# Kernel tuning notes

Measured on AMD Instinct MI355X. Metric: run time of the kernel, lower is better.

## Reference

```python
import jax, jax.numpy as jnp
import numpy as np

EPSILON = 1e-6
B, I, H, C, S = 131072, 64, 128, 16, 3  # batch, input_size, hidden_size, num_channels, spatial dim


def _linear_w(key, fan_in, fan_out):
    # torch.nn.Linear default init: U(-1/sqrt(fan_in), 1/sqrt(fan_in)); stored as [in, out] for x @ W
    bound = 1.0 / np.sqrt(fan_in)
    return jax.random.uniform(key, (fan_in, fan_out), jnp.float32, -bound, bound)


def setup_inputs() -> dict:
    key = jax.random.key(0)
    ks = jax.random.split(key, 11)
    return {
        "invariant_input": jax.random.normal(ks[0], (B, I), jnp.float32),
        "equivariant_input": jax.random.normal(ks[1], (B, S), jnp.float32),
        "invariant_hidden": jax.random.normal(ks[2], (B, H), jnp.float32),
        "equivariant_hidden": jax.random.normal(ks[3], (B, S, C), jnp.float32),
        # DotProductProjection(1+C -> H), no bias
        "W_left": _linear_w(ks[4], 1 + C, H),
        "W_right": _linear_w(ks[5], 1 + C, H),
        # invariant_to_invariant: Linear(I+H -> H) with bias
        "W_ii": _linear_w(ks[6], I + H, H),
        "b_ii": jax.random.uniform(ks[7], (H,), jnp.float32, -1.0 / np.sqrt(I + H), 1.0 / np.sqrt(I + H)),
        # equivariant_to_equivariant: Linear(1+C -> C), no bias
        "W_ee": _linear_w(ks[8], 1 + C, C),
        # Damping fc: Linear(I+H -> C), no bias
        "W_damp": _linear_w(ks[9], I + H, C),
    }


def reference(invariant_input, equivariant_input, invariant_hidden, equivariant_hidden,
              W_left, W_right, W_ii, b_ii, W_ee, W_damp):
    # eq_comb: [B, S, 1+C]; inv_comb: [B, I+H]
    eq_comb = jnp.concatenate([equivariant_input[..., None], equivariant_hidden], axis=-1)
    inv_comb = jnp.concatenate([invariant_input, invariant_hidden], axis=-1)

    # DotProductProjection (x1 = x0): normalize by squared-norm over spatial dim, project, dot over spatial dim
    norm = jnp.sum(eq_comb * eq_comb, axis=-2, keepdims=True) + EPSILON  # [B, 1, 1+C]
    xn = eq_comb / norm                                                  # [B, S, 1+C]
    proj = jnp.sum((xn @ W_left) * (xn @ W_right), axis=-2)              # [B, H]

    new_invariant = jnp.tanh(proj + inv_comb @ W_ii + b_ii)              # [B, H]

    # Damping: equivariant state gated by an invariant-derived per-channel factor
    gate = (inv_comb @ W_damp)[..., None, :]                             # [B, 1, C]
    new_equivariant = eq_comb @ W_ee + equivariant_hidden * gate         # [B, S, C]

    return (new_invariant, new_equivariant)
```

## Files before the change

kernel.cpp:

```cpp
#include <hip/hip_runtime.h>


typedef _Float16 half8  __attribute__((ext_vector_type(8)));
typedef _Float16 half4v __attribute__((ext_vector_type(4)));
typedef float    float4v __attribute__((ext_vector_type(4)));

#define MFMA16(A, Bv, C) __builtin_amdgcn_mfma_f32_16x16x32_f16((A), (Bv), (C), 0, 0, 0)

#define N_TILES 8192
#define GRID    2048

__global__ __launch_bounds__(256, 2) void rye_elman_kernel(
    const float* __restrict__ inv_in,
    const float* __restrict__ eq_in,
    const float* __restrict__ inv_hid,
    const float* __restrict__ eq_hid,
    const float* __restrict__ Wl_g,
    const float* __restrict__ Wr_g,
    const float* __restrict__ Wii_g,
    const float* __restrict__ bii_g,
    const float* __restrict__ Wee_g,
    const float* __restrict__ Wd_g,
    float* __restrict__ out0,
    float* __restrict__ out1)
{
    __shared__ __align__(16) _Float16 A_ii[16][200];
    __shared__ __align__(16) _Float16 A_xn[16][136];
    __shared__ __align__(16) _Float16 A_rw[16][136];
    __shared__ float eqin_s[16][3];
    __shared__ __align__(16) float eh_s[16][48];
    __shared__ __align__(16) float proj_s[16][132];
    __shared__ float ee_s[16][52];
    __shared__ float gate_s[16][16];

    const int tid  = threadIdx.x;
    const int w    = tid >> 6;
    const int lane = tid & 63;
    const int q    = lane >> 4;
    const int m    = lane & 15;

    {
        unsigned* z0 = (unsigned*)&A_xn[0][0];
        unsigned* z1 = (unsigned*)&A_rw[0][0];
        for (int i = tid; i < 16 * 136 / 2; i += 256) { z0[i] = 0u; z1[i] = 0u; }
    }

    half8 wii[2][6], wl[2], wr[2], wdamp[6], wee;
    float biiv[2];
#pragma unroll
    for (int t = 0; t < 2; ++t) {
        const int col = 32 * w + 16 * t + m;
        biiv[t] = bii_g[col];
#pragma unroll
        for (int s = 0; s < 6; ++s) {
            half8 u;
#pragma unroll
            for (int j = 0; j < 8; ++j)
                u[j] = (_Float16)Wii_g[(32 * s + 8 * q + j) * 128 + col];
            wii[t][s] = u;
        }
        half8 ul, ur;
#pragma unroll
        for (int j = 0; j < 8; ++j) {
            const int k = 8 * q + j;
            ul[j] = (k < 17) ? (_Float16)Wl_g[k * 128 + col] : (_Float16)0.f;
            ur[j] = (k < 17) ? (_Float16)Wr_g[k * 128 + col] : (_Float16)0.f;
        }
        wl[t] = ul; wr[t] = ur;
    }
#pragma unroll
    for (int s = 0; s < 6; ++s) {
        half8 u;
#pragma unroll
        for (int j = 0; j < 8; ++j)
            u[j] = (_Float16)Wd_g[(32 * s + 8 * q + j) * 16 + m];
        wdamp[s] = u;
    }
    {
        half8 u;
#pragma unroll
        for (int j = 0; j < 8; ++j) {
            const int k = 8 * q + j;
            u[j] = (k < 17) ? (_Float16)Wee_g[k * 16 + m] : (_Float16)0.f;
        }
        wee = u;
    }
    __syncthreads();

    float4 p_inv, p_hid0, p_hid1, p_eh;
    float  p_eq;

#define LOAD_TILE(BASE)                                                     \
    do {                                                                    \
        const long _b = (BASE);                                             \
        p_inv  = ((const float4*)(inv_in  + _b * 64))[tid];                 \
        p_hid0 = ((const float4*)(inv_hid + _b * 128))[tid];                \
        p_hid1 = ((const float4*)(inv_hid + _b * 128))[tid + 256];          \
        if (tid < 192) p_eh = ((const float4*)(eq_hid + _b * 48))[tid];     \
        if (tid < 48)  p_eq = eq_in[_b * 3 + tid];                          \
    } while (0)

    LOAD_TILE((long)blockIdx.x * 16);

    for (int tile = blockIdx.x; tile < N_TILES; tile += GRID) {
        const long base = (long)tile * 16;

        if (tid < 48) eqin_s[tid / 3][tid % 3] = p_eq;
        if (tid < 192) *(float4*)&eh_s[tid / 12][(tid % 12) * 4] = p_eh;
        {
            half4v h; h[0] = (_Float16)p_inv.x; h[1] = (_Float16)p_inv.y;
                      h[2] = (_Float16)p_inv.z; h[3] = (_Float16)p_inv.w;
            *(half4v*)&A_ii[tid >> 4][(tid & 15) * 4] = h;
        }
        {
            half4v h; h[0] = (_Float16)p_hid0.x; h[1] = (_Float16)p_hid0.y;
                      h[2] = (_Float16)p_hid0.z; h[3] = (_Float16)p_hid0.w;
            *(half4v*)&A_ii[tid >> 5][64 + (tid & 31) * 4] = h;
            const int i1 = tid + 256;
            half4v g; g[0] = (_Float16)p_hid1.x; g[1] = (_Float16)p_hid1.y;
                      g[2] = (_Float16)p_hid1.z; g[3] = (_Float16)p_hid1.w;
            *(half4v*)&A_ii[i1 >> 5][64 + (i1 & 31) * 4] = g;
        }
        __syncthreads();

        if (tile + GRID < N_TILES) LOAD_TILE((long)(tile + GRID) * 16);

        for (int t = tid; t < 816; t += 256) {
            const int r = t / 51, rem = t % 51;
            const int s = rem / 17, c = rem % 17;
            float x0, x1, x2;
            if (c == 0) { x0 = eqin_s[r][0]; x1 = eqin_s[r][1]; x2 = eqin_s[r][2]; }
            else        { x0 = eh_s[r][c - 1]; x1 = eh_s[r][15 + c]; x2 = eh_s[r][31 + c]; }
            const float a  = fmaf(x0, x0, fmaf(x1, x1, fmaf(x2, x2, 1e-6f)));
            const float rn = __builtin_amdgcn_rcpf(a);
            const float x  = (s == 0) ? x0 : (s == 1) ? x1 : x2;
            A_rw[r][s * 32 + c] = (_Float16)x;
            A_xn[r][s * 32 + c] = (_Float16)(x * rn);
        }
        __syncthreads();

        float4v acc[2] = {{0.f,0.f,0.f,0.f},{0.f,0.f,0.f,0.f}};
        float4v accg   = {0.f,0.f,0.f,0.f};
#pragma unroll
        for (int s = 0; s < 6; ++s) {
            half8 a = *(const half8*)&A_ii[m][8 * q + 32 * s];
            acc[0] = MFMA16(a, wii[0][s], acc[0]);
            acc[1] = MFMA16(a, wii[1][s], acc[1]);
            if (w == 0) accg = MFMA16(a, wdamp[s], accg);
        }
        const float4v z4 = {0.f,0.f,0.f,0.f};
#pragma unroll
        for (int g = 0; g < 4; ++g) {
            const int arow = 4 * g + (m >> 2);
            const int aoff = (m & 3) * 32 + 8 * q;
            half8 ax = *(const half8*)&A_xn[arow][aoff];
#pragma unroll
            for (int t = 0; t < 2; ++t) {
                float4v L = MFMA16(ax, wl[t], z4);
                float4v R = MFMA16(ax, wr[t], z4);
                proj_s[4 * g + q][32 * w + 16 * t + m] =
                    L[0]*R[0] + L[1]*R[1] + L[2]*R[2];
            }
            if (w == 1) {
                half8 ar = *(const half8*)&A_rw[arow][aoff];
                float4v E = MFMA16(ar, wee, z4);
                ee_s[4 * g + q][m]      = E[0];
                ee_s[4 * g + q][16 + m] = E[1];
                ee_s[4 * g + q][32 + m] = E[2];
            }
        }
        if (w == 0) {
#pragma unroll
            for (int r = 0; r < 4; ++r) gate_s[4 * q + r][m] = accg[r];
        }
        __syncthreads();

#pragma unroll
        for (int t = 0; t < 2; ++t) {
            const int col = 32 * w + 16 * t + m;
#pragma unroll
            for (int r = 0; r < 4; ++r) {
                const float x = acc[t][r] + proj_s[4 * q + r][col] + biiv[t];
                const float e = __expf(2.f * x);
                proj_s[4 * q + r][col] = 1.f - 2.f * __builtin_amdgcn_rcpf(e + 1.f);
            }
        }
        for (int i = tid; i < 768; i += 256) {
            const int b = i / 48, j = i % 48;
            out1[base * 48 + i] = ee_s[b][j] + eh_s[b][j] * gate_s[b][j & 15];
        }
        __syncthreads();

        {
            const long ob = base * 128;
#pragma unroll
            for (int h = 0; h < 2; ++h) {
                const int idx = (tid + 256 * h) * 4;
                const int r = idx >> 7, c = idx & 127;
                float4 v = *(const float4*)&proj_s[r][c];
                *(float4*)&out0[ob + idx] = v;
            }
        }
    }
#undef LOAD_TILE
}

extern "C" void kernel_launch(void* const* d_in, const int* in_sizes, int n_in,
                              void* d_out, int out_size, void* d_ws, size_t ws_size,
                              hipStream_t stream) {
    const float* inv_in  = (const float*)d_in[0];
    const float* eq_in   = (const float*)d_in[1];
    const float* inv_hid = (const float*)d_in[2];
    const float* eq_hid  = (const float*)d_in[3];
    const float* Wl      = (const float*)d_in[4];
    const float* Wr      = (const float*)d_in[5];
    const float* Wii     = (const float*)d_in[6];
    const float* bii     = (const float*)d_in[7];
    const float* Wee     = (const float*)d_in[8];
    const float* Wd      = (const float*)d_in[9];
    float* o0 = (float*)d_out;
    float* o1 = o0 + (size_t)131072 * 128;
    hipLaunchKernelGGL(rye_elman_kernel, dim3(GRID), dim3(256), 0, stream,
                       inv_in, eq_in, inv_hid, eq_hid, Wl, Wr, Wii, bii, Wee, Wd, o0, o1);
}
```

Before: 247.1 us.

## Restructure to one wave per 16-row tile with weights staged in LDS

Each wave now processes its own 16-row tile. The weights are converted to fp16 once per block and held in transposed, padded LDS buffers instead of registers. Activations are loaded straight from global memory into MFMA operand registers, which removes the per-tile LDS staging and all block-level barriers inside the tile loop. Outputs are written directly from the MFMA results, trading coalesced float4 stores for scattered scalar stores and dropping the software prefetch of the next tile. The block size becomes 512 threads with a grid of 512 blocks.

```diff
diff --git a/kernel.cpp b/kernel.cpp
--- a/kernel.cpp
+++ b/kernel.cpp
@@ -2,15 +2,17 @@
 
 
 typedef _Float16 half8  __attribute__((ext_vector_type(8)));
-typedef _Float16 half4v __attribute__((ext_vector_type(4)));
 typedef float    float4v __attribute__((ext_vector_type(4)));
 
-#define MFMA16(A, Bv, C) __builtin_amdgcn_mfma_f32_16x16x32_f16((A), (Bv), (C), 0, 0, 0)
+#define MFMA16(A, B, C) __builtin_amdgcn_mfma_f32_16x16x32_f16((A), (B), (C), 0, 0, 0)
 
-#define N_TILES 8192
-#define GRID    2048
+#define WII_P 200
+#define WLR_P 40
+#define NTILES 8192
+#define NBLOCKS 512
+#define NWAVES (NBLOCKS * 8)
 
-__global__ __launch_bounds__(256, 2) void rye_elman_kernel(
+__global__ __launch_bounds__(512, 4) void rye_elman_kernel(
     const float* __restrict__ inv_in,
     const float* __restrict__ eq_in,
     const float* __restrict__ inv_hid,
@@ -24,185 +26,155 @@
     float* __restrict__ out0,
     float* __restrict__ out1)
 {
-    __shared__ __align__(16) _Float16 A_ii[16][200];
-    __shared__ __align__(16) _Float16 A_xn[16][136];
-    __shared__ __align__(16) _Float16 A_rw[16][136];
-    __shared__ float eqin_s[16][3];
-    __shared__ __align__(16) float eh_s[16][48];
-    __shared__ __align__(16) float proj_s[16][132];
-    __shared__ float ee_s[16][52];
-    __shared__ float gate_s[16][16];
+    __shared__ __align__(16) _Float16 Wii_t[128 * WII_P];
+    __shared__ __align__(16) _Float16 Wl_t [128 * WLR_P];
+    __shared__ __align__(16) _Float16 Wr_t [128 * WLR_P];
+    __shared__ __align__(16) _Float16 Wd_t [ 16 * WII_P];
+    __shared__ __align__(16) _Float16 We_t [ 16 * WLR_P];
+    __shared__ float bii_s[128];
 
-    const int tid  = threadIdx.x;
-    const int w    = tid >> 6;
+    const int tid = threadIdx.x;
+
+    for (int i = tid; i < 128 * WLR_P; i += 512) { Wl_t[i] = (_Float16)0.f; Wr_t[i] = (_Float16)0.f; }
+    for (int i = tid; i < 16 * WLR_P; i += 512)  We_t[i] = (_Float16)0.f;
+    __syncthreads();
+    for (int i = tid; i < 192 * 128; i += 512) {
+        const int k = i >> 7, c = i & 127;
+        Wii_t[c * WII_P + k] = (_Float16)Wii_g[i];
+    }
+    for (int i = tid; i < 17 * 128; i += 512) {
+        const int r = i >> 7, c = i & 127, sl = (r == 0) ? 16 : r - 1;
+        Wl_t[c * WLR_P + sl] = (_Float16)Wl_g[i];
+        Wr_t[c * WLR_P + sl] = (_Float16)Wr_g[i];
+    }
+    for (int i = tid; i < 192 * 16; i += 512) {
+        const int k = i >> 4, c = i & 15;
+        Wd_t[c * WII_P + k] = (_Float16)Wd_g[i];
+    }
+    for (int i = tid; i < 17 * 16; i += 512) {
+        const int r = i >> 4, c = i & 15, sl = (r == 0) ? 16 : r - 1;
+        We_t[c * WLR_P + sl] = (_Float16)Wee_g[i];
+    }
+    if (tid < 128) bii_s[tid] = bii_g[tid];
+    __syncthreads();
+
     const int lane = tid & 63;
     const int q    = lane >> 4;
     const int m    = lane & 15;
+    const int wgid = (blockIdx.x << 3) + (tid >> 6);
 
-    {
-        unsigned* z0 = (unsigned*)&A_xn[0][0];
-        unsigned* z1 = (unsigned*)&A_rw[0][0];
-        for (int i = tid; i < 16 * 136 / 2; i += 256) { z0[i] = 0u; z1[i] = 0u; }
-    }
+    for (int tile = wgid; tile < NTILES; tile += NWAVES) {
+        const long base = (long)tile << 4;
+        const long rowm = base + m;
 
-    half8 wii[2][6], wl[2], wr[2], wdamp[6], wee;
-    float biiv[2];
+        float4 av[6][2];
+        {
+            const float4* pi = (const float4*)(inv_in  + rowm * 64);
+            const float4* ph = (const float4*)(inv_hid + rowm * 128);
 #pragma unroll
-    for (int t = 0; t < 2; ++t) {
-        const int col = 32 * w + 16 * t + m;
-        biiv[t] = bii_g[col];
+            for (int s = 0; s < 2; ++s) { av[s][0] = pi[8 * s + 2 * q]; av[s][1] = pi[8 * s + 2 * q + 1]; }
+#pragma unroll
+            for (int s = 0; s < 4; ++s) { av[s + 2][0] = ph[8 * s + 2 * q]; av[s + 2][1] = ph[8 * s + 2 * q + 1]; }
+        }
+        float xq[3][8];
+#pragma unroll
+        for (int s = 0; s < 3; ++s)
+#pragma unroll
+            for (int j = 0; j < 8; ++j) xq[s][j] = 0.f;
+        if (q < 2) {
+            const float4* pe = (const float4*)(eq_hid + rowm * 48);
+#pragma unroll
+            for (int s = 0; s < 3; ++s) {
+                const float4 u0 = pe[4 * s + 2 * q], u1 = pe[4 * s + 2 * q + 1];
+                xq[s][0] = u0.x; xq[s][1] = u0.y; xq[s][2] = u0.z; xq[s][3] = u0.w;
+                xq[s][4] = u1.x; xq[s][5] = u1.y; xq[s][6] = u1.z; xq[s][7] = u1.w;
+            }
+        } else if (q == 2) {
+#pragma unroll
+            for (int s = 0; s < 3; ++s) xq[s][0] = eq_in[rowm * 3 + s];
+        }
+
+        half8 aii[6];
 #pragma unroll
         for (int s = 0; s < 6; ++s) {
-            half8 u;
-#pragma unroll
-            for (int j = 0; j < 8; ++j)
-                u[j] = (_Float16)Wii_g[(32 * s + 8 * q + j) * 128 + col];
-            wii[t][s] = u;
+            half8 h;
+            h[0] = (_Float16)av[s][0].x; h[1] = (_Float16)av[s][0].y;
+            h[2] = (_Float16)av[s][0].z; h[3] = (_Float16)av[s][0].w;
+            h[4] = (_Float16)av[s][1].x; h[5] = (_Float16)av[s][1].y;
+            h[6] = (_Float16)av[s][1].z; h[7] = (_Float16)av[s][1].w;
+            aii[s] = h;
         }
-        half8 ul, ur;
+        float rn[8];
 #pragma unroll
         for (int j = 0; j < 8; ++j) {
-            const int k = 8 * q + j;
-            ul[j] = (k < 17) ? (_Float16)Wl_g[k * 128 + col] : (_Float16)0.f;
-            ur[j] = (k < 17) ? (_Float16)Wr_g[k * 128 + col] : (_Float16)0.f;
+            const float nn = fmaf(xq[0][j], xq[0][j],
+                             fmaf(xq[1][j], xq[1][j],
+                             fmaf(xq[2][j], xq[2][j], 1e-6f)));
+            rn[j] = __builtin_amdgcn_rcpf(nn);
         }
-        wl[t] = ul; wr[t] = ur;
-    }
+        half8 xr[3], xnh[3];
 #pragma unroll
-    for (int s = 0; s < 6; ++s) {
-        half8 u;
+        for (int s = 0; s < 3; ++s) {
+            half8 hr, hn;
 #pragma unroll
-        for (int j = 0; j < 8; ++j)
-            u[j] = (_Float16)Wd_g[(32 * s + 8 * q + j) * 16 + m];
-        wdamp[s] = u;
-    }
-    {
-        half8 u;
+            for (int j = 0; j < 8; ++j) {
+                hr[j] = (_Float16)xq[s][j];
+                hn[j] = (_Float16)(xq[s][j] * rn[j]);
+            }
+            xr[s] = hr; xnh[s] = hn;
+        }
+
+        float4v acc[8];
 #pragma unroll
-        for (int j = 0; j < 8; ++j) {
-            const int k = 8 * q + j;
-            u[j] = (k < 17) ? (_Float16)Wee_g[k * 16 + m] : (_Float16)0.f;
-        }
-        wee = u;
-    }
-    __syncthreads();
-
-    float4 p_inv, p_hid0, p_hid1, p_eh;
-    float  p_eq;
-
-#define LOAD_TILE(BASE)                                                     \
-    do {                                                                    \
-        const long _b = (BASE);                                             \
-        p_inv  = ((const float4*)(inv_in  + _b * 64))[tid];                 \
-        p_hid0 = ((const float4*)(inv_hid + _b * 128))[tid];                \
-        p_hid1 = ((const float4*)(inv_hid + _b * 128))[tid + 256];          \
-        if (tid < 192) p_eh = ((const float4*)(eq_hid + _b * 48))[tid];     \
-        if (tid < 48)  p_eq = eq_in[_b * 3 + tid];                          \
-    } while (0)
-
-    LOAD_TILE((long)blockIdx.x * 16);
-
-    for (int tile = blockIdx.x; tile < N_TILES; tile += GRID) {
-        const long base = (long)tile * 16;
-
-        if (tid < 48) eqin_s[tid / 3][tid % 3] = p_eq;
-        if (tid < 192) *(float4*)&eh_s[tid / 12][(tid % 12) * 4] = p_eh;
-        {
-            half4v h; h[0] = (_Float16)p_inv.x; h[1] = (_Float16)p_inv.y;
-                      h[2] = (_Float16)p_inv.z; h[3] = (_Float16)p_inv.w;
-            *(half4v*)&A_ii[tid >> 4][(tid & 15) * 4] = h;
-        }
-        {
-            half4v h; h[0] = (_Float16)p_hid0.x; h[1] = (_Float16)p_hid0.y;
-                      h[2] = (_Float16)p_hid0.z; h[3] = (_Float16)p_hid0.w;
-            *(half4v*)&A_ii[tid >> 5][64 + (tid & 31) * 4] = h;
-            const int i1 = tid + 256;
-            half4v g; g[0] = (_Float16)p_hid1.x; g[1] = (_Float16)p_hid1.y;
-                      g[2] = (_Float16)p_hid1.z; g[3] = (_Float16)p_hid1.w;
-            *(half4v*)&A_ii[i1 >> 5][64 + (i1 & 31) * 4] = g;
-        }
-        __syncthreads();
-
-        if (tile + GRID < N_TILES) LOAD_TILE((long)(tile + GRID) * 16);
-
-        for (int t = tid; t < 816; t += 256) {
-            const int r = t / 51, rem = t % 51;
-            const int s = rem / 17, c = rem % 17;
-            float x0, x1, x2;
-            if (c == 0) { x0 = eqin_s[r][0]; x1 = eqin_s[r][1]; x2 = eqin_s[r][2]; }
-            else        { x0 = eh_s[r][c - 1]; x1 = eh_s[r][15 + c]; x2 = eh_s[r][31 + c]; }
-            const float a  = fmaf(x0, x0, fmaf(x1, x1, fmaf(x2, x2, 1e-6f)));
-            const float rn = __builtin_amdgcn_rcpf(a);
-            const float x  = (s == 0) ? x0 : (s == 1) ? x1 : x2;
-            A_rw[r][s * 32 + c] = (_Float16)x;
-            A_xn[r][s * 32 + c] = (_Float16)(x * rn);
-        }
-        __syncthreads();
-
-        float4v acc[2] = {{0.f,0.f,0.f,0.f},{0.f,0.f,0.f,0.f}};
-        float4v accg   = {0.f,0.f,0.f,0.f};
+        for (int t = 0; t < 8; ++t) acc[t] = (float4v){0.f, 0.f, 0.f, 0.f};
+        float4v gacc = (float4v){0.f, 0.f, 0.f, 0.f};
 #pragma unroll
         for (int s = 0; s < 6; ++s) {
-            half8 a = *(const half8*)&A_ii[m][8 * q + 32 * s];
-            acc[0] = MFMA16(a, wii[0][s], acc[0]);
-            acc[1] = MFMA16(a, wii[1][s], acc[1]);
-            if (w == 0) accg = MFMA16(a, wdamp[s], accg);
+            const int ko = 32 * s + 8 * q;
+            gacc = MFMA16(aii[s], *(const half8*)&Wd_t[m * WII_P + ko], gacc);
+#pragma unroll
+            for (int t = 0; t < 8; ++t)
+                acc[t] = MFMA16(aii[s], *(const half8*)&Wii_t[(16 * t + m) * WII_P + ko], acc[t]);
         }
-        const float4v z4 = {0.f,0.f,0.f,0.f};
+
+        const float4v z4 = (float4v){0.f, 0.f, 0.f, 0.f};
 #pragma unroll
-        for (int g = 0; g < 4; ++g) {
-            const int arow = 4 * g + (m >> 2);
-            const int aoff = (m & 3) * 32 + 8 * q;
-            half8 ax = *(const half8*)&A_xn[arow][aoff];
+        for (int t = 0; t < 8; ++t) {
+            const int col = 16 * t + m;
+            const half8 bl = *(const half8*)&Wl_t[col * WLR_P + 8 * q];
+            const half8 br = *(const half8*)&Wr_t[col * WLR_P + 8 * q];
+            const float4v L0 = MFMA16(xnh[0], bl, z4);
+            const float4v R0 = MFMA16(xnh[0], br, z4);
+            const float4v L1 = MFMA16(xnh[1], bl, z4);
+            const float4v R1 = MFMA16(xnh[1], br, z4);
+            const float4v L2 = MFMA16(xnh[2], bl, z4);
+            const float4v R2 = MFMA16(xnh[2], br, z4);
+            const float bb = bii_s[col];
 #pragma unroll
-            for (int t = 0; t < 2; ++t) {
-                float4v L = MFMA16(ax, wl[t], z4);
-                float4v R = MFMA16(ax, wr[t], z4);
-                proj_s[4 * g + q][32 * w + 16 * t + m] =
-                    L[0]*R[0] + L[1]*R[1] + L[2]*R[2];
-            }
-            if (w == 1) {
-                half8 ar = *(const half8*)&A_rw[arow][aoff];
-                float4v E = MFMA16(ar, wee, z4);
-                ee_s[4 * g + q][m]      = E[0];
-                ee_s[4 * g + q][16 + m] = E[1];
-                ee_s[4 * g + q][32 + m] = E[2];
+            for (int r = 0; r < 4; ++r) {
+                const float pr = L0[r] * R0[r] + L1[r] * R1[r] + L2[r] * R2[r];
+                const float x  = acc[t][r] + pr + bb;
+                const float e  = __expf(2.f * x);
+                out0[(base + 4 * q + r) * 128 + col] = 1.f - 2.f * __builtin_amdgcn_rcpf(e + 1.f);
             }
         }
-        if (w == 0) {
-#pragma unroll
-            for (int r = 0; r < 4; ++r) gate_s[4 * q + r][m] = accg[r];
-        }
-        __syncthreads();
 
-#pragma unroll
-        for (int t = 0; t < 2; ++t) {
-            const int col = 32 * w + 16 * t + m;
+        {
+            const half8 be = *(const half8*)&We_t[m * WLR_P + 8 * q];
+            const float4v E0 = MFMA16(xr[0], be, z4);
+            const float4v E1 = MFMA16(xr[1], be, z4);
+            const float4v E2 = MFMA16(xr[2], be, z4);
 #pragma unroll
             for (int r = 0; r < 4; ++r) {
-                const float x = acc[t][r] + proj_s[4 * q + r][col] + biiv[t];
-                const float e = __expf(2.f * x);
-                proj_s[4 * q + r][col] = 1.f - 2.f * __builtin_amdgcn_rcpf(e + 1.f);
-            }
-        }
-        for (int i = tid; i < 768; i += 256) {
-            const int b = i / 48, j = i % 48;
-            out1[base * 48 + i] = ee_s[b][j] + eh_s[b][j] * gate_s[b][j & 15];
-        }
-        __syncthreads();
-
-        {
-            const long ob = base * 128;
-#pragma unroll
-            for (int h = 0; h < 2; ++h) {
-                const int idx = (tid + 256 * h) * 4;
-                const int r = idx >> 7, c = idx & 127;
-                float4 v = *(const float4*)&proj_s[r][c];
-                *(float4*)&out0[ob + idx] = v;
+                const long  rw = base + 4 * q + r;
+                const float g  = gacc[r];
+                const float* eh = eq_hid + rw * 48 + m;
+                out1[rw * 48 +      m] = E0[r] + eh[0]  * g;
+                out1[rw * 48 + 16 + m] = E1[r] + eh[16] * g;
+                out1[rw * 48 + 32 + m] = E2[r] + eh[32] * g;
             }
         }
     }
-#undef LOAD_TILE
 }
 
 extern "C" void kernel_launch(void* const* d_in, const int* in_sizes, int n_in,
@@ -220,6 +192,6 @@
     const float* Wd      = (const float*)d_in[9];
     float* o0 = (float*)d_out;
     float* o1 = o0 + (size_t)131072 * 128;
-    hipLaunchKernelGGL(rye_elman_kernel, dim3(GRID), dim3(256), 0, stream,
+    hipLaunchKernelGGL(rye_elman_kernel, dim3(NBLOCKS), dim3(512), 0, stream,
                        inv_in, eq_in, inv_hid, eq_hid, Wl, Wr, Wii, bii, Wee, Wd, o0, o1);
 }
```

New measurement: 411.5 us. 66.6% more time.
